# Performance work log

Hardware: AMD Instinct MI355X
Metric: run time of the kernel (lower is better)

## Reference

```python
import jax, jax.numpy as jnp
import numpy as np

B, S, D = 2, 512, 128      # batch, seq_len, d_att
DG, NG = 64, 2             # d_group, n_group = D // DG


def setup_inputs() -> dict:
    key = jax.random.key(0)
    ks = jax.random.split(key, 12)
    def w(k, shape, scale):
        return jax.random.normal(k, shape, dtype=jnp.float32) * scale
    proj_scale = 1.0 / D                      # xavier_uniform-ish std / sqrt(d_att)
    mlp1 = (2.0 / (DG + DG)) ** 0.5
    mlp2 = (2.0 / (DG + 16)) ** 0.5
    mlp3 = (2.0 / (16 + 1)) ** 0.5
    return {
        "x": w(ks[0], (B, S, D), 1.0),
        "positional_adding_bias": w(ks[1], (1, NG, 1, S, S), 1.0),
        "positional_multiplying_bias": jax.random.uniform(ks[2], (1, NG, 1, S, S), dtype=jnp.float32),
        "Wq": w(ks[3], (D, D), proj_scale),
        "Wk": w(ks[4], (D, D), proj_scale),
        "Wv": w(ks[5], (D, D), proj_scale),
        "W1": w(ks[6], (DG, DG), mlp1), "b1": jnp.zeros((DG,), jnp.float32),
        "W2": w(ks[7], (DG, 16), mlp2), "b2": jnp.zeros((16,), jnp.float32),
        "W3": w(ks[8], (16, 1), mlp3),  "b3": jnp.zeros((1,), jnp.float32),
    }


def reference(x, positional_adding_bias, positional_multiplying_bias,
              Wq, Wk, Wv, W1, b1, W2, b2, W3, b3):
    Q = x @ Wq   # [B,S,D]
    K = x @ Wk
    V = x @ Wv
    # pairwise Q-K differences, grouped: [B,S,S,NG,DG] (d_att split as n_group,d_group)
    diff = (Q[:, :, None, :] - K[:, None, :, :]).reshape(B, S, S, NG, DG)
    # per-group scoring MLP (Linear->ReLU x3, final width 1)
    h = jax.nn.relu(diff @ W1 + b1)
    h = jax.nn.relu(h @ W2 + b2)
    a = jax.nn.relu(h @ W3 + b3)                 # [B,S,S,NG,1]
    a = jnp.transpose(a, (0, 3, 4, 1, 2))        # [B,NG,1,S,S]
    a = a * positional_multiplying_bias + positional_adding_bias
    a = jax.nn.softmax(a, axis=-1)[:, :, 0]      # [B,NG,S,S], softmax over keys
    # NOTE: original reshapes V as (d_group, n_group) — faithful reproduction
    Vr = V.reshape(B, S, DG, NG)                 # [B,S,DG,NG]
    out = jnp.einsum('bisk,bkji->bsji', a, Vr)   # [B,S,DG,NG]
    return out.reshape(B, S, D)
```

## Files before the change

### kernel.cpp

```cpp
#include <hip/hip_runtime.h>

#define BQ 2
#define SQ 512
#define DQ 128
#define DGQ 64
#define NGQ 2

typedef float f32x4 __attribute__((ext_vector_type(4)));
typedef __bf16 bf16x8 __attribute__((ext_vector_type(8)));


__global__ __launch_bounds__(256) void proj_kernel(
    const float* __restrict__ x,
    const float* __restrict__ Wq, const float* __restrict__ Wk,
    const float* __restrict__ Wv,
    const float* __restrict__ W1, const float* __restrict__ b1,
    float* __restrict__ QW1, float* __restrict__ KW1, float* __restrict__ Vp)
{
    const int t = threadIdx.x;
    const int row = blockIdx.x;
    __shared__ float xs[DQ];
    __shared__ float part[3][2][DQ];
    __shared__ float qs[DQ], ks[DQ];

    if (t < DQ) xs[t] = x[(size_t)row * DQ + t];
    __syncthreads();

    const int f = t & 127, h = t >> 7;
    float aq = 0.f, ak = 0.f, av = 0.f;
    const int d0 = h * 64;
    #pragma unroll 8
    for (int d = 0; d < 64; ++d) {
        const float xv = xs[d0 + d];
        const size_t o = (size_t)(d0 + d) * DQ + f;
        aq = fmaf(xv, Wq[o], aq);
        ak = fmaf(xv, Wk[o], ak);
        av = fmaf(xv, Wv[o], av);
    }
    part[0][h][f] = aq; part[1][h][f] = ak; part[2][h][f] = av;
    __syncthreads();

    if (t < DQ) {
        qs[t] = part[0][0][t] + part[0][1][t];
        const float v = part[2][0][t] + part[2][1][t];
        Vp[((size_t)row * NGQ + (t & 1)) * DGQ + (t >> 1)] = v;
    } else {
        const int f2 = t - DQ;
        ks[f2] = part[1][0][f2] + part[1][1][f2];
    }
    __syncthreads();

    const int fb = t & 127, side = t >> 7;
    const int g = fb >> 6, c = fb & 63;
    const float* src = side ? ks : qs;
    float acc = side ? 0.f : b1[c];
    #pragma unroll 8
    for (int e = 0; e < 64; ++e)
        acc = fmaf(src[g * 64 + e], W1[e * DGQ + c], acc);
    (side ? KW1 : QW1)[(size_t)row * DQ + fb] = acc;
}

__global__ __launch_bounds__(512, 4) void attn_kernel(
    const float* __restrict__ QW1, const float* __restrict__ KW1,
    const float* __restrict__ Vp,
    const float* __restrict__ W2, const float* __restrict__ b2,
    const float* __restrict__ W3, const float* __restrict__ b3,
    const float* __restrict__ pos_add, const float* __restrict__ pos_mul,
    float* __restrict__ out)
{
    const int t = threadIdx.x;
    const int lane = t & 63, w = t >> 6;
    const int lg = lane >> 4, lr = lane & 15;
    const int ib = blockIdx.x & 127;
    const int g  = (blockIdx.x >> 7) & 1;
    const int b  = blockIdx.x >> 8;
    const int i0 = ib * 4;

    __shared__ __align__(16) float Qs[4][DGQ];
    __shared__ __align__(16) float logits[4][SQ];
    __shared__ __align__(16) float pbuf[SQ * 4];
    __shared__ __align__(16) float avs[8][DGQ][4];
    __shared__ float redm[4][2], reds[4][2];

    if (t < 256) {
        const int i = t >> 6, k = t & 63;
        Qs[i][k] = QW1[((size_t)(b * SQ + i0 + i)) * DQ + g * DGQ + k];
    }

    bf16x8 bhf[2], blf[2];
    #pragma unroll
    for (int H = 0; H < 2; ++H) {
        #pragma unroll
        for (int e = 0; e < 8; ++e) {
            const int k = H * 32 + (e >> 2) * 16 + lg * 4 + (e & 3);
            const float wv = W2[k * 16 + lr];
            const __bf16 hi = (__bf16)wv;
            bhf[H][e] = hi;
            blf[H][e] = (__bf16)(wv - (float)hi);
        }
    }
    const float w3r = W3[lr];
    const float b2r = b2[lr];
    const float b3s = b3[0];

    __syncthreads();

    #pragma unroll
    for (int pass = 0; pass < 2; ++pass) {
        const int jb0 = w * 64 + pass * 32;
        f32x4 kreg[2][4];
        #pragma unroll
        for (int u = 0; u < 2; ++u) {
            const float* kr =
                KW1 + ((size_t)(b * SQ + jb0 + u * 16 + lr)) * DQ + g * DGQ;
            #pragma unroll
            for (int c = 0; c < 4; ++c)
                kreg[u][c] = *reinterpret_cast<const f32x4*>(
                    kr + (c & 1) * 16 + (c >> 1) * 32 + lg * 4);
        }
        #pragma unroll
        for (int i = 0; i < 4; ++i) {
            f32x4 qf[4];
            #pragma unroll
            for (int c = 0; c < 4; ++c)
                qf[c] = *reinterpret_cast<const f32x4*>(
                    &Qs[i][(c & 1) * 16 + (c >> 1) * 32 + lg * 4]);
            #pragma unroll
            for (int u = 0; u < 2; ++u) {
                f32x4 acc = {0.f, 0.f, 0.f, 0.f};
                #pragma unroll
                for (int H = 0; H < 2; ++H) {
                    bf16x8 ah, al;
                    #pragma unroll
                    for (int cc = 0; cc < 2; ++cc) {
                        const int c = H * 2 + cc;
                        #pragma unroll
                        for (int e = 0; e < 4; ++e) {
                            const float hv =
                                fmaxf(qf[c][e] - kreg[u][c][e], 0.f);
                            const __bf16 hb = (__bf16)hv;
                            ah[cc * 4 + e] = hb;
                            al[cc * 4 + e] = (__bf16)(hv - (float)hb);
                        }
                    }
                    acc = __builtin_amdgcn_mfma_f32_16x16x32_bf16(
                        ah, bhf[H], acc, 0, 0, 0);
                    acc = __builtin_amdgcn_mfma_f32_16x16x32_bf16(
                        al, bhf[H], acc, 0, 0, 0);
                    acc = __builtin_amdgcn_mfma_f32_16x16x32_bf16(
                        ah, blf[H], acc, 0, 0, 0);
                }
                float s0 = fmaxf(acc[0] + b2r, 0.f) * w3r;
                float s1 = fmaxf(acc[1] + b2r, 0.f) * w3r;
                float s2 = fmaxf(acc[2] + b2r, 0.f) * w3r;
                float s3 = fmaxf(acc[3] + b2r, 0.f) * w3r;
                #pragma unroll
                for (int off = 1; off < 16; off <<= 1) {
                    s0 += __shfl_xor(s0, off);
                    s1 += __shfl_xor(s1, off);
                    s2 += __shfl_xor(s2, off);
                    s3 += __shfl_xor(s3, off);
                }
                if (lr == 0) {
                    f32x4 sv = {s0, s1, s2, s3};
                    *reinterpret_cast<f32x4*>(
                        &logits[i][jb0 + u * 16 + lg * 4]) = sv;
                }
            }
        }
    }
    __syncthreads();

    const int si = w >> 1, hf = w & 1;
    const int qi = i0 + si;
    const int j0 = hf * 256 + lane * 4;
    const f32x4 raw = *reinterpret_cast<const f32x4*>(&logits[si][j0]);
    const size_t po = ((size_t)(g * SQ + qi)) * SQ + j0;
    const f32x4 pm4 = *reinterpret_cast<const f32x4*>(pos_mul + po);
    const f32x4 pa4 = *reinterpret_cast<const f32x4*>(pos_add + po);
    f32x4 lgt;
    #pragma unroll
    for (int c = 0; c < 4; ++c)
        lgt[c] = fmaf(fmaxf(raw[c] + b3s, 0.f), pm4[c], pa4[c]);
    float m = fmaxf(fmaxf(lgt[0], lgt[1]), fmaxf(lgt[2], lgt[3]));
    #pragma unroll
    for (int off = 1; off < 64; off <<= 1) m = fmaxf(m, __shfl_xor(m, off));
    if (lane == 0) redm[si][hf] = m;
    __syncthreads();
    const float M = fmaxf(redm[si][0], redm[si][1]);
    f32x4 e4;
    float ls = 0.f;
    #pragma unroll
    for (int c = 0; c < 4; ++c) { e4[c] = __expf(lgt[c] - M); ls += e4[c]; }
    #pragma unroll
    for (int c = 0; c < 4; ++c) pbuf[(j0 + c) * 4 + si] = e4[c];
    #pragma unroll
    for (int off = 1; off < 64; off <<= 1) ls += __shfl_xor(ls, off);
    if (lane == 0) reds[si][hf] = ls;
    __syncthreads();

    f32x4 av = {0.f, 0.f, 0.f, 0.f};
    const float* vb =
        Vp + (((size_t)(b * SQ + w * 64)) * NGQ + g) * DGQ + lane;
    #pragma unroll 8
    for (int n = 0; n < 64; ++n) {
        const float v = vb[(size_t)n * (NGQ * DGQ)];
        const f32x4 p4 =
            *reinterpret_cast<const f32x4*>(&pbuf[(w * 64 + n) * 4]);
        av += v * p4;
    }
    *reinterpret_cast<f32x4*>(&avs[w][lane][0]) = av;
    __syncthreads();

    if (t < 256) {
        const int i2 = t >> 6, d = t & 63;
        float sum = 0.f;
        #pragma unroll
        for (int ww = 0; ww < 8; ++ww) sum += avs[ww][d][i2];
        const float den = reds[i2][0] + reds[i2][1];
        out[((size_t)(b * SQ + i0 + i2)) * DQ + d * NGQ + g] = sum / den;
    }
}

extern "C" void kernel_launch(void* const* d_in, const int* in_sizes, int n_in,
                              void* d_out, int out_size, void* d_ws, size_t ws_size,
                              hipStream_t stream) {
    const float* x       = (const float*)d_in[0];
    const float* pos_add = (const float*)d_in[1];
    const float* pos_mul = (const float*)d_in[2];
    const float* Wq      = (const float*)d_in[3];
    const float* Wk      = (const float*)d_in[4];
    const float* Wv      = (const float*)d_in[5];
    const float* W1      = (const float*)d_in[6];
    const float* b1      = (const float*)d_in[7];
    const float* W2      = (const float*)d_in[8];
    const float* b2      = (const float*)d_in[9];
    const float* W3      = (const float*)d_in[10];
    const float* b3      = (const float*)d_in[11];
    float* out = (float*)d_out;

    float* ws  = (float*)d_ws;
    float* QW1 = ws;
    float* KW1 = ws + 131072;
    float* Vp  = ws + 262144;

    proj_kernel<<<BQ * SQ, 256, 0, stream>>>(x, Wq, Wk, Wv, W1, b1,
                                             QW1, KW1, Vp);
    attn_kernel<<<BQ * NGQ * SQ / 4, 512, 0, stream>>>(QW1, KW1, Vp, W2, b2,
                                                       W3, b3, pos_add, pos_mul,
                                                       out);
}
```

Measured before the change: 112.3 us.

## Process more query rows per block and swap MFMA operands to shrink reductions

The projection kernel now handles four rows per 512-thread block, reusing each weight load across rows. The attention kernel handles eight query rows per block instead of four, so each K tile loaded into registers is reused across twice as many queries. The MFMA operand order is swapped so the W2 hidden dimension lands across the accumulator elements, which replaces the four-value 16-lane shuffle reduction with a per-lane FMA and two shuffles. The softmax is reorganised so each thread covers one key across all eight queries. This halves the grid and lowers the occupancy hint in the launch bounds, which may reduce latency hiding and load balance across CUs.

Result: slower. 115.3 us (+2.7%).

```diff
diff --git a/kernel.cpp b/kernel.cpp
--- a/kernel.cpp
+++ b/kernel.cpp
@@ -10,7 +10,7 @@
 typedef __bf16 bf16x8 __attribute__((ext_vector_type(8)));
 
 
-__global__ __launch_bounds__(256) void proj_kernel(
+__global__ __launch_bounds__(512) void proj_kernel(
     const float* __restrict__ x,
     const float* __restrict__ Wq, const float* __restrict__ Wk,
     const float* __restrict__ Wv,
@@ -18,49 +18,78 @@
     float* __restrict__ QW1, float* __restrict__ KW1, float* __restrict__ Vp)
 {
     const int t = threadIdx.x;
-    const int row = blockIdx.x;
-    __shared__ float xs[DQ];
-    __shared__ float part[3][2][DQ];
-    __shared__ float qs[DQ], ks[DQ];
-
-    if (t < DQ) xs[t] = x[(size_t)row * DQ + t];
+    const int row0 = blockIdx.x * 4;
+    __shared__ float xs[4][DQ];
+    __shared__ float part[3][4][4][DQ];
+    __shared__ float qs[4][DQ], ks[4][DQ];
+
+    ((float*)xs)[t] = x[(size_t)row0 * DQ + t];
     __syncthreads();
 
     const int f = t & 127, h = t >> 7;
-    float aq = 0.f, ak = 0.f, av = 0.f;
-    const int d0 = h * 64;
+    const int d0 = h * 32;
+    float aq[4] = {0.f, 0.f, 0.f, 0.f};
+    float ak[4] = {0.f, 0.f, 0.f, 0.f};
+    float av[4] = {0.f, 0.f, 0.f, 0.f};
     #pragma unroll 8
-    for (int d = 0; d < 64; ++d) {
-        const float xv = xs[d0 + d];
+    for (int d = 0; d < 32; ++d) {
         const size_t o = (size_t)(d0 + d) * DQ + f;
-        aq = fmaf(xv, Wq[o], aq);
-        ak = fmaf(xv, Wk[o], ak);
-        av = fmaf(xv, Wv[o], av);
-    }
-    part[0][h][f] = aq; part[1][h][f] = ak; part[2][h][f] = av;
-    __syncthreads();
-
-    if (t < DQ) {
-        qs[t] = part[0][0][t] + part[0][1][t];
-        const float v = part[2][0][t] + part[2][1][t];
-        Vp[((size_t)row * NGQ + (t & 1)) * DGQ + (t >> 1)] = v;
-    } else {
-        const int f2 = t - DQ;
-        ks[f2] = part[1][0][f2] + part[1][1][f2];
-    }
-    __syncthreads();
-
-    const int fb = t & 127, side = t >> 7;
+        const float wq = Wq[o], wk = Wk[o], wv = Wv[o];
+        #pragma unroll
+        for (int r = 0; r < 4; ++r) {
+            const float xv = xs[r][d0 + d];
+            aq[r] = fmaf(xv, wq, aq[r]);
+            ak[r] = fmaf(xv, wk, ak[r]);
+            av[r] = fmaf(xv, wv, av[r]);
+        }
+    }
+    #pragma unroll
+    for (int r = 0; r < 4; ++r) {
+        part[0][h][r][f] = aq[r];
+        part[1][h][r][f] = ak[r];
+        part[2][h][r][f] = av[r];
+    }
+    __syncthreads();
+
+    const int fc = t & 127, sel = t >> 7;
+    if (sel == 0) {
+        #pragma unroll
+        for (int r = 0; r < 4; ++r)
+            qs[r][fc] = part[0][0][r][fc] + part[0][1][r][fc] +
+                        part[0][2][r][fc] + part[0][3][r][fc];
+    } else if (sel == 1) {
+        #pragma unroll
+        for (int r = 0; r < 4; ++r)
+            ks[r][fc] = part[1][0][r][fc] + part[1][1][r][fc] +
+                        part[1][2][r][fc] + part[1][3][r][fc];
+    } else if (sel == 2) {
+        #pragma unroll
+        for (int r = 0; r < 4; ++r) {
+            const float v = part[2][0][r][fc] + part[2][1][r][fc] +
+                            part[2][2][r][fc] + part[2][3][r][fc];
+            Vp[((size_t)(row0 + r) * NGQ + (fc & 1)) * DGQ + (fc >> 1)] = v;
+        }
+    }
+    __syncthreads();
+
+    const int fb = t & 127, rp = (t >> 7) & 1, side = t >> 8;
     const int g = fb >> 6, c = fb & 63;
-    const float* src = side ? ks : qs;
-    float acc = side ? 0.f : b1[c];
+    const float* src = side ? &ks[0][0] : &qs[0][0];
+    const int r0 = rp * 2;
+    float a0 = side ? 0.f : b1[c];
+    float a1 = a0;
     #pragma unroll 8
-    for (int e = 0; e < 64; ++e)
-        acc = fmaf(src[g * 64 + e], W1[e * DGQ + c], acc);
-    (side ? KW1 : QW1)[(size_t)row * DQ + fb] = acc;
+    for (int e = 0; e < 64; ++e) {
+        const float w1v = W1[e * DGQ + c];
+        a0 = fmaf(src[r0 * DQ + g * 64 + e], w1v, a0);
+        a1 = fmaf(src[(r0 + 1) * DQ + g * 64 + e], w1v, a1);
+    }
+    float* dst = side ? KW1 : QW1;
+    dst[(size_t)(row0 + r0) * DQ + fb] = a0;
+    dst[(size_t)(row0 + r0 + 1) * DQ + fb] = a1;
 }
 
-__global__ __launch_bounds__(512, 4) void attn_kernel(
+__global__ __launch_bounds__(512, 2) void attn_kernel(
     const float* __restrict__ QW1, const float* __restrict__ KW1,
     const float* __restrict__ Vp,
     const float* __restrict__ W2, const float* __restrict__ b2,
@@ -71,21 +100,19 @@
     const int t = threadIdx.x;
     const int lane = t & 63, w = t >> 6;
     const int lg = lane >> 4, lr = lane & 15;
-    const int ib = blockIdx.x & 127;
-    const int g  = (blockIdx.x >> 7) & 1;
-    const int b  = blockIdx.x >> 8;
-    const int i0 = ib * 4;
-
-    __shared__ __align__(16) float Qs[4][DGQ];
-    __shared__ __align__(16) float logits[4][SQ];
-    __shared__ __align__(16) float pbuf[SQ * 4];
-    __shared__ __align__(16) float avs[8][DGQ][4];
-    __shared__ float redm[4][2], reds[4][2];
-
-    if (t < 256) {
-        const int i = t >> 6, k = t & 63;
-        Qs[i][k] = QW1[((size_t)(b * SQ + i0 + i)) * DQ + g * DGQ + k];
-    }
+    const int ib = blockIdx.x & 63;
+    const int g  = (blockIdx.x >> 6) & 1;
+    const int b  = blockIdx.x >> 7;
+    const int i0 = ib * 8;
+
+    __shared__ __align__(16) float Qs[8][DGQ];
+    __shared__ __align__(16) float logits[8][SQ];
+    __shared__ __align__(16) float pbuf[SQ][8];
+    __shared__ __align__(16) float avs[8][8][DGQ];
+    __shared__ float redm[8][8], reds[8][8];
+
+    Qs[t >> 6][t & 63] = QW1[((size_t)(b * SQ + i0 + (t >> 6))) * DQ +
+                             g * DGQ + (t & 63)];
 
     bf16x8 bhf[2], blf[2];
     #pragma unroll
@@ -99,9 +126,14 @@
             blf[H][e] = (__bf16)(wv - (float)hi);
         }
     }
-    const float w3r = W3[lr];
-    const float b2r = b2[lr];
+    float b2c[4], w3c[4];
+    #pragma unroll
+    for (int r = 0; r < 4; ++r) {
+        b2c[r] = b2[lg * 4 + r];
+        w3c[r] = W3[lg * 4 + r];
+    }
     const float b3s = b3[0];
+    const f32x4 zero4 = {0.f, 0.f, 0.f, 0.f};
 
     __syncthreads();
 
@@ -119,7 +151,7 @@
                     kr + (c & 1) * 16 + (c >> 1) * 32 + lg * 4);
         }
         #pragma unroll
-        for (int i = 0; i < 4; ++i) {
+        for (int i = 0; i < 8; ++i) {
             f32x4 qf[4];
             #pragma unroll
             for (int c = 0; c < 4; ++c)
@@ -127,99 +159,110 @@
                     &Qs[i][(c & 1) * 16 + (c >> 1) * 32 + lg * 4]);
             #pragma unroll
             for (int u = 0; u < 2; ++u) {
-                f32x4 acc = {0.f, 0.f, 0.f, 0.f};
+                f32x4 acc = zero4;
                 #pragma unroll
                 for (int H = 0; H < 2; ++H) {
+                    f32x4 dd0 = qf[H * 2]     - kreg[u][H * 2];
+                    f32x4 dd1 = qf[H * 2 + 1] - kreg[u][H * 2 + 1];
+                    dd0 = __builtin_elementwise_max(dd0, zero4);
+                    dd1 = __builtin_elementwise_max(dd1, zero4);
                     bf16x8 ah, al;
                     #pragma unroll
-                    for (int cc = 0; cc < 2; ++cc) {
-                        const int c = H * 2 + cc;
-                        #pragma unroll
-                        for (int e = 0; e < 4; ++e) {
-                            const float hv =
-                                fmaxf(qf[c][e] - kreg[u][c][e], 0.f);
-                            const __bf16 hb = (__bf16)hv;
-                            ah[cc * 4 + e] = hb;
-                            al[cc * 4 + e] = (__bf16)(hv - (float)hb);
-                        }
+                    for (int e = 0; e < 4; ++e) {
+                        const __bf16 hb = (__bf16)dd0[e];
+                        ah[e] = hb;
+                        al[e] = (__bf16)(dd0[e] - (float)hb);
+                    }
+                    #pragma unroll
+                    for (int e = 0; e < 4; ++e) {
+                        const __bf16 hb = (__bf16)dd1[e];
+                        ah[4 + e] = hb;
+                        al[4 + e] = (__bf16)(dd1[e] - (float)hb);
                     }
                     acc = __builtin_amdgcn_mfma_f32_16x16x32_bf16(
-                        ah, bhf[H], acc, 0, 0, 0);
+                        bhf[H], ah, acc, 0, 0, 0);
                     acc = __builtin_amdgcn_mfma_f32_16x16x32_bf16(
-                        al, bhf[H], acc, 0, 0, 0);
+                        blf[H], ah, acc, 0, 0, 0);
                     acc = __builtin_amdgcn_mfma_f32_16x16x32_bf16(
-                        ah, blf[H], acc, 0, 0, 0);
+                        bhf[H], al, acc, 0, 0, 0);
                 }
-                float s0 = fmaxf(acc[0] + b2r, 0.f) * w3r;
-                float s1 = fmaxf(acc[1] + b2r, 0.f) * w3r;
-                float s2 = fmaxf(acc[2] + b2r, 0.f) * w3r;
-                float s3 = fmaxf(acc[3] + b2r, 0.f) * w3r;
+                float s = 0.f;
                 #pragma unroll
-                for (int off = 1; off < 16; off <<= 1) {
-                    s0 += __shfl_xor(s0, off);
-                    s1 += __shfl_xor(s1, off);
-                    s2 += __shfl_xor(s2, off);
-                    s3 += __shfl_xor(s3, off);
-                }
-                if (lr == 0) {
-                    f32x4 sv = {s0, s1, s2, s3};
-                    *reinterpret_cast<f32x4*>(
-                        &logits[i][jb0 + u * 16 + lg * 4]) = sv;
-                }
+                for (int r = 0; r < 4; ++r)
+                    s = fmaf(fmaxf(acc[r] + b2c[r], 0.f), w3c[r], s);
+                s += __shfl_xor(s, 16);
+                s += __shfl_xor(s, 32);
+                if (lg == 0) logits[i][jb0 + u * 16 + lr] = s;
             }
         }
     }
     __syncthreads();
 
-    const int si = w >> 1, hf = w & 1;
-    const int qi = i0 + si;
-    const int j0 = hf * 256 + lane * 4;
-    const f32x4 raw = *reinterpret_cast<const f32x4*>(&logits[si][j0]);
-    const size_t po = ((size_t)(g * SQ + qi)) * SQ + j0;
-    const f32x4 pm4 = *reinterpret_cast<const f32x4*>(pos_mul + po);
-    const f32x4 pa4 = *reinterpret_cast<const f32x4*>(pos_add + po);
-    f32x4 lgt;
-    #pragma unroll
-    for (int c = 0; c < 4; ++c)
-        lgt[c] = fmaf(fmaxf(raw[c] + b3s, 0.f), pm4[c], pa4[c]);
-    float m = fmaxf(fmaxf(lgt[0], lgt[1]), fmaxf(lgt[2], lgt[3]));
-    #pragma unroll
-    for (int off = 1; off < 64; off <<= 1) m = fmaxf(m, __shfl_xor(m, off));
-    if (lane == 0) redm[si][hf] = m;
-    __syncthreads();
-    const float M = fmaxf(redm[si][0], redm[si][1]);
-    f32x4 e4;
-    float ls = 0.f;
-    #pragma unroll
-    for (int c = 0; c < 4; ++c) { e4[c] = __expf(lgt[c] - M); ls += e4[c]; }
-    #pragma unroll
-    for (int c = 0; c < 4; ++c) pbuf[(j0 + c) * 4 + si] = e4[c];
-    #pragma unroll
-    for (int off = 1; off < 64; off <<= 1) ls += __shfl_xor(ls, off);
-    if (lane == 0) reds[si][hf] = ls;
-    __syncthreads();
-
-    f32x4 av = {0.f, 0.f, 0.f, 0.f};
+    const int jj = w * 64 + lane;
+    float lgv[8];
+    #pragma unroll
+    for (int q = 0; q < 8; ++q) {
+        const float raw = logits[q][jj];
+        const size_t po = ((size_t)(g * SQ + i0 + q)) * SQ + jj;
+        lgv[q] = fmaf(fmaxf(raw + b3s, 0.f), pos_mul[po], pos_add[po]);
+    }
+    #pragma unroll
+    for (int q = 0; q < 8; ++q) {
+        float m = lgv[q];
+        #pragma unroll
+        for (int off = 1; off < 64; off <<= 1)
+            m = fmaxf(m, __shfl_xor(m, off));
+        if (lane == 0) redm[q][w] = m;
+    }
+    __syncthreads();
+    float Mq[8];
+    #pragma unroll
+    for (int q = 0; q < 8; ++q) {
+        float M = redm[q][0];
+        #pragma unroll
+        for (int ww = 1; ww < 8; ++ww) M = fmaxf(M, redm[q][ww]);
+        Mq[q] = M;
+    }
+    float e8[8];
+    #pragma unroll
+    for (int q = 0; q < 8; ++q) e8[q] = __expf(lgv[q] - Mq[q]);
+    *reinterpret_cast<f32x4*>(&pbuf[jj][0]) = f32x4{e8[0], e8[1], e8[2], e8[3]};
+    *reinterpret_cast<f32x4*>(&pbuf[jj][4]) = f32x4{e8[4], e8[5], e8[6], e8[7]};
+    #pragma unroll
+    for (int q = 0; q < 8; ++q) {
+        float s = e8[q];
+        #pragma unroll
+        for (int off = 1; off < 64; off <<= 1) s += __shfl_xor(s, off);
+        if (lane == 0) reds[q][w] = s;
+    }
+    __syncthreads();
+
+    f32x4 a0 = zero4, a1 = zero4;
     const float* vb =
         Vp + (((size_t)(b * SQ + w * 64)) * NGQ + g) * DGQ + lane;
     #pragma unroll 8
     for (int n = 0; n < 64; ++n) {
         const float v = vb[(size_t)n * (NGQ * DGQ)];
-        const f32x4 p4 =
-            *reinterpret_cast<const f32x4*>(&pbuf[(w * 64 + n) * 4]);
-        av += v * p4;
-    }
-    *reinterpret_cast<f32x4*>(&avs[w][lane][0]) = av;
-    __syncthreads();
-
-    if (t < 256) {
-        const int i2 = t >> 6, d = t & 63;
-        float sum = 0.f;
-        #pragma unroll
-        for (int ww = 0; ww < 8; ++ww) sum += avs[ww][d][i2];
-        const float den = reds[i2][0] + reds[i2][1];
-        out[((size_t)(b * SQ + i0 + i2)) * DQ + d * NGQ + g] = sum / den;
-    }
+        const f32x4 p0 = *reinterpret_cast<const f32x4*>(&pbuf[w * 64 + n][0]);
+        const f32x4 p1 = *reinterpret_cast<const f32x4*>(&pbuf[w * 64 + n][4]);
+        a0 += v * p0;
+        a1 += v * p1;
+    }
+    #pragma unroll
+    for (int c = 0; c < 4; ++c) {
+        avs[w][c][lane]     = a0[c];
+        avs[w][4 + c][lane] = a1[c];
+    }
+    __syncthreads();
+
+    const int q = t >> 6, d = t & 63;
+    float sum = 0.f, den = 0.f;
+    #pragma unroll
+    for (int ww = 0; ww < 8; ++ww) {
+        sum += avs[ww][q][d];
+        den += reds[q][ww];
+    }
+    out[((size_t)(b * SQ + i0 + q)) * DQ + d * NGQ + g] = sum / den;
 }
 
 extern "C" void kernel_launch(void* const* d_in, const int* in_sizes, int n_in,
@@ -244,9 +287,9 @@
     float* KW1 = ws + 131072;
     float* Vp  = ws + 262144;
 
-    proj_kernel<<<BQ * SQ, 256, 0, stream>>>(x, Wq, Wk, Wv, W1, b1,
-                                             QW1, KW1, Vp);
-    attn_kernel<<<BQ * NGQ * SQ / 4, 512, 0, stream>>>(QW1, KW1, Vp, W2, b2,
+    proj_kernel<<<BQ * SQ / 4, 512, 0, stream>>>(x, Wq, Wk, Wv, W1, b1,
+                                                 QW1, KW1, Vp);
+    attn_kernel<<<BQ * NGQ * SQ / 8, 512, 0, stream>>>(QW1, KW1, Vp, W2, b2,
                                                        W3, b3, pos_add, pos_mul,
                                                        out);
 }
```
